# Kernel tuning notes

Measured on AMD Instinct MI355X. Metric: run time of the kernel, lower is better.

## Reference

```python
import jax, jax.numpy as jnp
import numpy as np

EMBED = 1024
HEADS = 16
HEAD_DIM = EMBED // HEADS
MAX_SEQ = 5000
THETA = 10000.0
BATCH = 16
SEQ_K = 1024
SEQ_Q = 512


def _rope_tables():
    inv = 1.0 / (THETA ** (np.arange(0, EMBED, 2)[: EMBED // 2] / EMBED))
    ang = np.outer(np.arange(MAX_SEQ), inv)  # [MAX_SEQ, EMBED//2]
    return jnp.asarray(np.cos(ang), jnp.float32), jnp.asarray(np.sin(ang), jnp.float32)

COS_T, SIN_T = _rope_tables()


def _apply_rope(x, idx):
    # x: [B, S, E]; idx: [B, S]; pairs are (x[...,2i], x[...,2i+1]) across the FULL embed dim
    B, S, E = x.shape
    xp = x.reshape(B, S, E // 2, 2)
    xr, xi = xp[..., 0], xp[..., 1]
    c, s = COS_T[idx], SIN_T[idx]  # [B, S, E//2]
    return jnp.stack([xr * c - xi * s, xr * s + xi * c], axis=-1).reshape(B, S, E)


def _attn_mask(key_padding_mask):
    # (causal triu OR key padding) AND NOT eye  (eye keeps diagonal attendable), then cut query rows
    tri = jnp.triu(jnp.ones((SEQ_K, SEQ_K), bool), k=1)
    m = jnp.logical_or(tri[None], key_padding_mask[:, None, :])  # [B, K, K]
    m = jnp.logical_and(m, ~jnp.eye(SEQ_K, dtype=bool)[None])
    return m[:, -SEQ_Q:, :]  # [B, Q, K]


def setup_inputs() -> dict:
    key = jax.random.key(0)
    ks = jax.random.split(key, 16)
    def lin(i):
        W = jax.random.normal(ks[i], (EMBED, EMBED), jnp.float32) / np.sqrt(EMBED).astype(np.float32)
        b = jnp.zeros((EMBED,), jnp.float32)
        return W, b
    Wq, bq = lin(0); Wk, bk = lin(1); Wv, bv = lin(2); Wo, bo = lin(3)
    Wxr, bxr = lin(4); Wyr, byr = lin(5)
    Wxz, bxz = lin(6); Wyz, byz = lin(7)
    Wxg, bxg = lin(8); Wyg, byg = lin(9)
    key_in = jax.random.normal(ks[10], (BATCH, SEQ_K, EMBED), jnp.float32)
    key_index = jnp.sort(jax.random.randint(ks[11], (BATCH, SEQ_K), 0, MAX_SEQ), axis=-1)
    key_padding_mask = jax.random.randint(ks[12], (BATCH, SEQ_K), 0, 2).astype(bool)
    return dict(key_in=key_in, key_index=key_index, key_padding_mask=key_padding_mask,
                Wq=Wq, bq=bq, Wk=Wk, bk=bk, Wv=Wv, bv=bv, Wo=Wo, bo=bo,
                Wxr=Wxr, bxr=bxr, Wyr=Wyr, byr=byr, Wxz=Wxz, bxz=bxz,
                Wyz=Wyz, byz=byz, Wxg=Wxg, bxg=bxg, Wyg=Wyg, byg=byg)


def reference(key_in, key_index, key_padding_mask,
              Wq, bq, Wk, bk, Wv, bv, Wo, bo,
              Wxr, bxr, Wyr, byr, Wxz, bxz, Wyz, byz, Wxg, bxg, Wyg, byg):
    B = key_in.shape[0]
    # cut_query=True: query is the last SEQ_Q steps of key
    query = key_in[:, -SEQ_Q:]
    q_idx = key_index[:, -SEQ_Q:]
    q = query @ Wq + bq
    k = key_in @ Wk + bk
    v = key_in @ Wv + bv
    # RoPE applied on full embed dim BEFORE head split (as in source)
    q = _apply_rope(q, q_idx)
    k = _apply_rope(k, key_index)
    qh = q.reshape(B, SEQ_Q, HEADS, HEAD_DIM)
    kh = k.reshape(B, SEQ_K, HEADS, HEAD_DIM)
    vh = v.reshape(B, SEQ_K, HEADS, HEAD_DIM)
    mask = _attn_mask(key_padding_mask)  # [B, Q, K]
    bias = jnp.where(mask, -jnp.inf, 0.0).astype(key_in.dtype)[:, None]  # [B,1,Q,K]
    scores = jnp.einsum('bqhd,bkhd->bhqk', qh, kh) / np.float32(np.sqrt(HEAD_DIM)) + bias
    w = jax.nn.softmax(scores, axis=-1)  # [B,H,Q,K]
    o = jnp.einsum('bhqk,bkhd->bqhd', w, vh).reshape(B, SEQ_Q, EMBED)
    o = o @ Wo + bo
    # GRU-style gated residual combine (use_residual=True, use_gated=True)
    x = query
    r = jax.nn.sigmoid(x @ Wxr + bxr + o @ Wyr + byr)
    z = jax.nn.sigmoid(x @ Wxz + bxz + o @ Wyz + byz)
    h = jnp.tanh((r * x) @ Wxg + bxg + o @ Wyg + byg)
    out = (1.0 - z) * x + z * h
    attn_weights = w.mean(axis=1)  # averaged over heads, [B, Q, K]
    return out, attn_weights
```

## Files before the change

kernel.cpp:

```cpp
#include <hip/hip_runtime.h>
#include <hip/hip_bf16.h>


typedef __attribute__((ext_vector_type(8))) short bf16x8;
typedef __attribute__((ext_vector_type(4))) float f32x4;

__device__ __forceinline__ short f2bs(float f) {
  union { __hip_bfloat16 h; short s; } u; u.h = __float2bfloat16(f); return u.s;
}

static constexpr size_t OFF_WT   = 0;
static constexpr size_t OFF_TAB  = 20971520;
static constexpr size_t OFF_XBF  = 41451520;
static constexpr size_t OFF_QH   = 75005952;
static constexpr size_t OFF_KH   = 91783168;
static constexpr size_t OFF_VT   = 125337600;
static constexpr size_t OFF_OAT  = 158892032;
static constexpr size_t OFF_O2   = 175669248;
static constexpr size_t OFF_INV  = OFF_OAT;
static constexpr size_t OFF_RBZB = 75005952;
static constexpr size_t OFF_RX   = 142114816;
static constexpr size_t OFF_HB   = OFF_XBF;

__device__ __forceinline__ int swz(int q) { return ((q & 3) << 3) ^ ((q & 12) << 2); }

__global__ __launch_bounds__(256) void k_cvtx(const float* __restrict__ x,
                                              short* __restrict__ xbf) {
  size_t i = ((size_t)blockIdx.x * 256 + threadIdx.x) * 8;
  f32x4 a = *(const f32x4*)(x + i);
  f32x4 b = *(const f32x4*)(x + i + 4);
  bf16x8 o;
  o[0] = f2bs(a[0]); o[1] = f2bs(a[1]); o[2] = f2bs(a[2]); o[3] = f2bs(a[3]);
  o[4] = f2bs(b[0]); o[5] = f2bs(b[1]); o[6] = f2bs(b[2]); o[7] = f2bs(b[3]);
  *(bf16x8*)(xbf + i) = o;
}

__global__ void k_tabinv(double* __restrict__ inv) {
  int i = threadIdx.x;
  inv[i] = pow(10000.0, -(double)i / 512.0);
}
__global__ __launch_bounds__(256) void k_table(float* __restrict__ tab,
                                               const double* __restrict__ inv) {
  int i = blockIdx.x * 256 + threadIdx.x;
  if (i >= 5000 * 512) return;
  int pos = i >> 9, fi = i & 511;
  double ds, dc;
  sincos((double)pos * inv[fi], &ds, &dc);
  tab[2 * i] = (float)dc;
  tab[2 * i + 1] = (float)ds;
}

struct W10 { const float* p[10]; };
__global__ __launch_bounds__(256) void k_wt(W10 wsrc, short* __restrict__ wt) {
  __shared__ short t[32][33];
  int kb = blockIdx.x * 32, nb = blockIdx.y * 32, wi = blockIdx.z;
  const float* src = wsrc.p[wi];
  int tid = threadIdx.x;
#pragma unroll
  for (int e = 0; e < 4; ++e) {
    int idx = e * 256 + tid;
    int kr = idx >> 5, nc = idx & 31;
    t[nc][kr] = f2bs(src[(size_t)(kb + kr) * 1024 + nb + nc]);
  }
  __syncthreads();
  short* dst = wt + (size_t)wi * 1024 * 1024;
#pragma unroll
  for (int e = 0; e < 4; ++e) {
    int idx = e * 256 + tid;
    int nr = idx >> 5, kc = idx & 31;
    dst[(size_t)(nb + nr) * 1024 + kb + kc] = t[nr][kc];
  }
}

enum { CM_BF16 = 0, CM_F32 = 2, CM_F32ACC = 3, CM_VT = 4, CM_ROPE = 5 };

template <int AMODE, int CMODE>
__global__ __launch_bounds__(256) void k_gemm(
    const short* __restrict__ A, const short* __restrict__ Bt,
    const float* __restrict__ bias, const float* __restrict__ bias2,
    void* __restrict__ Cout, int ldc,
    const float* __restrict__ tab, const int* __restrict__ kidx,
    int sshift, int qoff) {
  __shared__ __align__(16) short lA[128 * 32];
  __shared__ __align__(16) short lB[128 * 32];
  const int tid = threadIdx.x;
  const int lane = tid & 63;
  const int wv = tid >> 6;
  const int wm = wv >> 1, wn = wv & 1;
  const int lo = lane & 15, hi = lane >> 4;
  const int tm0 = blockIdx.x * 128;
  const int tn0 = blockIdx.y * 128;

  const f32x4 vz = {0.f, 0.f, 0.f, 0.f};
  f32x4 acc[4][4];
#pragma unroll
  for (int m = 0; m < 4; ++m)
#pragma unroll
    for (int n = 0; n < 4; ++n) acc[m][n] = vz;

  for (int kt = 0; kt < 32; ++kt) {
    const int k0 = kt * 32;
    __syncthreads();
#pragma unroll
    for (int i = 0; i < 2; ++i) {
      int f = i * 256 + tid;
      int r = f >> 2;
      int cb = (f & 3) * 16;
      int arow = tm0 + r;
      if (AMODE) arow = ((arow >> 9) << 10) + 512 + (arow & 511);
      const char* ga = (const char*)(A + (size_t)arow * 1024 + k0) + cb;
      __builtin_amdgcn_global_load_lds(
          (const __attribute__((address_space(1))) void*)ga,
          (__attribute__((address_space(3))) void*)((char*)lA + (size_t)(i * 256 + wv * 64) * 16),
          16, 0, 0);
      int brow = tn0 + r;
      const char* gb = (const char*)(Bt + (size_t)brow * 1024 + k0) + cb;
      __builtin_amdgcn_global_load_lds(
          (const __attribute__((address_space(1))) void*)gb,
          (__attribute__((address_space(3))) void*)((char*)lB + (size_t)(i * 256 + wv * 64) * 16),
          16, 0, 0);
    }
    __syncthreads();
    bf16x8 af[4], bfr[4];
#pragma unroll
    for (int m = 0; m < 4; ++m)
      af[m] = *(const bf16x8*)&lA[(wm * 64 + m * 16 + lo) * 32 + hi * 8];
#pragma unroll
    for (int n = 0; n < 4; ++n)
      bfr[n] = *(const bf16x8*)&lB[(wn * 64 + n * 16 + lo) * 32 + hi * 8];
#pragma unroll
    for (int m = 0; m < 4; ++m)
#pragma unroll
      for (int n = 0; n < 4; ++n)
        acc[m][n] = __builtin_amdgcn_mfma_f32_16x16x32_bf16(af[m], bfr[n], acc[m][n], 0, 0, 0);
  }

  if constexpr (CMODE == CM_ROPE) {
    __hip_bfloat16* out = (__hip_bfloat16*)Cout;
    const float2* t2 = (const float2*)tab;
    const int srows = 1 << sshift;
    const float sgn = (lane & 1) ? 1.f : -1.f;
#pragma unroll
    for (int m = 0; m < 4; ++m) {
      int row_base = tm0 + wm * 64 + m * 16 + hi * 4;
#pragma unroll
      for (int n = 0; n < 4; ++n) {
        int col = tn0 + wn * 64 + n * 16 + lo;
        float bsv = bias[col];
        int j = col >> 1, hh = col >> 6, dd = col & 63;
#pragma unroll
        for (int r = 0; r < 4; ++r) {
          int row = row_base + r;
          int bb = row >> sshift, ss = row & (srows - 1);
          int idx = kidx[bb * 1024 + qoff + ss];
          float2 cs = t2[(size_t)idx * 512 + j];
          float val = acc[m][n][r] + bsv;
          float part = __shfl_xor(val, 1);
          float rot = val * cs.x + sgn * part * cs.y;
          out[((size_t)(bb * 16 + hh) * srows + ss) * 64 + dd] = __float2bfloat16(rot);
        }
      }
    }
  } else if constexpr (CMODE == CM_VT) {
    __hip_bfloat16* out = (__hip_bfloat16*)Cout;
#pragma unroll
    for (int m = 0; m < 4; ++m) {
      int row_base = tm0 + wm * 64 + m * 16 + hi * 4;
#pragma unroll
      for (int n = 0; n < 4; ++n) {
        int col = tn0 + wn * 64 + n * 16 + lo;
        float bsv = bias[col];
        int hh = col >> 6, dd = col & 63;
#pragma unroll
        for (int r = 0; r < 4; ++r) {
          int row = row_base + r;
          int bb = row >> 10, ss = row & 1023;
          out[((size_t)(bb * 16 + hh) * 64 + dd) * 1024 + ss] =
              __float2bfloat16(acc[m][n][r] + bsv);
        }
      }
    }
  } else if constexpr (CMODE == CM_F32 || CMODE == CM_F32ACC) {
    float* out = (float*)Cout;
#pragma unroll
    for (int m = 0; m < 4; ++m) {
      int row_base = tm0 + wm * 64 + m * 16 + hi * 4;
#pragma unroll
      for (int n = 0; n < 4; ++n) {
        int col = tn0 + wn * 64 + n * 16 + lo;
        float bsv = (col < 1024 || !bias2) ? bias[col] : bias2[col - 1024];
#pragma unroll
        for (int r = 0; r < 4; ++r) {
          size_t off = (size_t)(row_base + r) * ldc + col;
          float val = acc[m][n][r] + bsv;
          if constexpr (CMODE == CM_F32ACC) val += out[off];
          out[off] = val;
        }
      }
    }
  } else {
    __hip_bfloat16* out = (__hip_bfloat16*)Cout;
#pragma unroll
    for (int m = 0; m < 4; ++m) {
      int row_base = tm0 + wm * 64 + m * 16 + hi * 4;
#pragma unroll
      for (int n = 0; n < 4; ++n) {
        int col = tn0 + wn * 64 + n * 16 + lo;
        float bsv = bias[col];
#pragma unroll
        for (int r = 0; r < 4; ++r) {
          size_t off = (size_t)(row_base + r) * ldc + col;
          out[off] = __float2bfloat16(acc[m][n][r] + bsv);
        }
      }
    }
  }
}

__global__ __launch_bounds__(512, 1) void k_attn(
    const __hip_bfloat16* __restrict__ qh,
    const __hip_bfloat16* __restrict__ kh,
    const __hip_bfloat16* __restrict__ vt,
    const unsigned char* __restrict__ padraw,
    float* __restrict__ mean_out,
    __hip_bfloat16* __restrict__ oat) {
  __shared__ float Sld[16 * 1024];
  short* Pld = (short*)Sld;
  const int wgid = blockIdx.x;
  const int b = wgid & 15, qt = wgid >> 4;
  const int tid = threadIdx.x, lane = tid & 63, wv = tid >> 6;
  const int lo = lane & 15, hi = lane >> 4;
  const int wg = wv & 3, half = wv >> 2;
  const f32x4 vz = {0.f, 0.f, 0.f, 0.f};

  auto oscw = [&](int idx) -> float& { return Sld[(idx >> 9) * 1024 + (idx & 511)]; };

  bool is_byte = false;
#pragma unroll
  for (int j = 1; j < 256; ++j)
    if ((j & 3) && padraw[j] == 1) is_byte = true;
  const int* ipad = (const int*)padraw;

  unsigned pmask = 0;
#pragma unroll
  for (int nt = 0; nt < 8; ++nt) {
    int kpos = wv * 128 + nt * 16 + lo;
    int pk = is_byte ? (int)padraw[b * 1024 + kpos]
                     : (ipad[b * 1024 + kpos] != 0 ? 1 : 0);
    pmask |= (unsigned)(pk != 0) << nt;
  }

  float macc[2][16];
#pragma unroll
  for (int rr = 0; rr < 2; ++rr)
#pragma unroll
    for (int i = 0; i < 16; ++i) macc[rr][i] = 0.f;

  const __hip_bfloat16* qbase =
      qh + ((size_t)(b * 16) * 512 + (size_t)qt * 16) * 64;
  bf16x8 qf0 = *(const bf16x8*)(qbase + (size_t)lo * 64 + hi * 8);
  bf16x8 qf1 = *(const bf16x8*)(qbase + (size_t)lo * 64 + 32 + hi * 8);

  bf16x8 kb0[8], kb1[8];
  {
    const __hip_bfloat16* kbh0 = kh + (size_t)(b * 16) * 1024 * 64;
#pragma unroll
    for (int p = 0; p < 8; ++p) {
      int kr = wv * 128 + p * 16 + lo;
      kb0[p] = *(const bf16x8*)(kbh0 + (size_t)kr * 64 + hi * 8);
      kb1[p] = *(const bf16x8*)(kbh0 + (size_t)kr * 64 + 32 + hi * 8);
    }
  }

  for (int h = 0; h < 16; ++h) {
    const __hip_bfloat16* vrow =
        vt + ((size_t)(b * 16 + h) * 64 + wg * 16 + lo) * 1024;
    const int kcg = half * 16;

    bf16x8 vbuf[16];
#pragma unroll
    for (int nt = 0; nt < 8; ++nt) {
      vbuf[2 * nt]     = *(const bf16x8*)(vrow + (kcg + 2 * nt) * 32 + hi * 8);
      vbuf[2 * nt + 1] = *(const bf16x8*)(vrow + (kcg + 2 * nt + 1) * 32 + hi * 8);
      f32x4 sa = vz;
      sa = __builtin_amdgcn_mfma_f32_16x16x32_bf16(qf0, kb0[nt], sa, 0, 0, 0);
      sa = __builtin_amdgcn_mfma_f32_16x16x32_bf16(qf1, kb1[nt], sa, 0, 0, 0);
      int kpos = wv * 128 + nt * 16 + lo;
      int pk = (pmask >> nt) & 1;
#pragma unroll
      for (int r = 0; r < 4; ++r) {
        int q = hi * 4 + r;
        int qg = 512 + qt * 16 + q;
        float sv = sa[r] * 0.125f;
        bool msk = (kpos > qg) || (kpos < qg && pk != 0);
        Sld[q * 1024 + (kpos ^ swz(q))] = msk ? -1e30f : sv;
      }
    }
    __syncthreads();

#pragma unroll
    for (int rr = 0; rr < 2; ++rr) {
      int q = wv * 2 + rr;
      const int c = swz(q);
      float* row = Sld + q * 1024;
      float v[16], mx = -1e30f;
#pragma unroll
      for (int i = 0; i < 16; ++i) {
        v[i] = row[(lane + i * 64) ^ c];
        mx = fmaxf(mx, v[i]);
      }
#pragma unroll
      for (int off = 32; off > 0; off >>= 1) mx = fmaxf(mx, __shfl_xor(mx, off));
      float sum = 0.f;
#pragma unroll
      for (int i = 0; i < 16; ++i) { v[i] = __expf(v[i] - mx); sum += v[i]; }
#pragma unroll
      for (int off = 32; off > 0; off >>= 1) sum += __shfl_xor(sum, off);
      float invs = 1.0f / sum;
      short* prow = Pld + q * 2048 + 1024;
#pragma unroll
      for (int i = 0; i < 16; ++i) {
        float p = v[i] * invs;
        prow[(lane + i * 64) ^ c] = f2bs(p);
        macc[rr][i] += p;
      }
    }
    __syncthreads();

    f32x4 oacc = vz;
    {
      const short* prow = Pld + lo * 2048 + 1024;
      const int cl = swz(lo);
      const __hip_bfloat16* kbn =
          kh + (size_t)(b * 16 + (h < 15 ? h + 1 : h)) * 1024 * 64;
#pragma unroll
      for (int kc = 0; kc < 16; ++kc) {
        if (kc < 8 && h < 15) {
          int kr = wv * 128 + kc * 16 + lo;
          kb0[kc] = *(const bf16x8*)(kbn + (size_t)kr * 64 + hi * 8);
          kb1[kc] = *(const bf16x8*)(kbn + (size_t)kr * 64 + 32 + hi * 8);
        }
        bf16x8 pa = *(const bf16x8*)&prow[((kcg + kc) * 32 + hi * 8) ^ cl];
        oacc = __builtin_amdgcn_mfma_f32_16x16x32_bf16(pa, vbuf[kc], oacc, 0, 0, 0);
      }
    }

    if (h < 15) {
      const __hip_bfloat16* qn = qbase + (size_t)(h + 1) * 512 * 64;
      qf0 = *(const bf16x8*)(qn + (size_t)lo * 64 + hi * 8);
      qf1 = *(const bf16x8*)(qn + (size_t)lo * 64 + 32 + hi * 8);
    }

    if (half == 1) {
#pragma unroll
      for (int r = 0; r < 4; ++r) oscw((wg * 64 + lane) * 4 + r) = oacc[r];
    }
    __syncthreads();
    if (half == 0) {
#pragma unroll
      for (int r = 0; r < 4; ++r) {
        float o = oacc[r] + oscw((wg * 64 + lane) * 4 + r);
        int q = qt * 16 + hi * 4 + r;
        oat[((size_t)b * 512 + q) * 1024 + h * 64 + wg * 16 + lo] =
            __float2bfloat16(o);
      }
    }
    __syncthreads();
  }

#pragma unroll
  for (int rr = 0; rr < 2; ++rr) {
    size_t mrow = ((size_t)b * 512 + (size_t)qt * 16 + wv * 2 + rr) * 1024;
#pragma unroll
    for (int i = 0; i < 16; ++i)
      mean_out[mrow + lane + i * 64] = macc[rr][i] * 0.0625f;
  }
}

__global__ __launch_bounds__(256) void k_rx(const float* __restrict__ RbZb,
                                            const float* __restrict__ x,
                                            short* __restrict__ rx) {
  size_t base = ((size_t)blockIdx.x * 256 + threadIdx.x) * 4;
  int row = (int)(base >> 10), col = (int)(base & 1023);
  int b = row >> 9, s = row & 511;
  const float* xp = x + ((size_t)(b * 1024 + 512 + s) << 10) + col;
  f32x4 rv = *(const f32x4*)(RbZb + (size_t)row * 2048 + col);
  f32x4 xv = *(const f32x4*)xp;
  typedef __attribute__((ext_vector_type(4))) short s16x4;
  s16x4 o;
#pragma unroll
  for (int j = 0; j < 4; ++j) {
    float r = 1.f / (1.f + __expf(-rv[j]));
    o[j] = f2bs(r * xv[j]);
  }
  *(s16x4*)(rx + base) = o;
}

__global__ __launch_bounds__(256) void k_final(const float* __restrict__ RbZb,
                                               const float* __restrict__ Hb,
                                               const float* __restrict__ x,
                                               float* __restrict__ out0) {
  size_t base = ((size_t)blockIdx.x * 256 + threadIdx.x) * 4;
  int row = (int)(base >> 10), col = (int)(base & 1023);
  int b = row >> 9, s = row & 511;
  const float* xp = x + ((size_t)(b * 1024 + 512 + s) << 10) + col;
  f32x4 zv = *(const f32x4*)(RbZb + (size_t)row * 2048 + 1024 + col);
  f32x4 hv = *(const f32x4*)(Hb + base);
  f32x4 xv = *(const f32x4*)xp;
  f32x4 o;
#pragma unroll
  for (int j = 0; j < 4; ++j) {
    float z = 1.f / (1.f + __expf(-zv[j]));
    float hh = tanhf(hv[j]);
    o[j] = (1.f - z) * xv[j] + z * hh;
  }
  *(f32x4*)(out0 + base) = o;
}

extern "C" void kernel_launch(void* const* d_in, const int* in_sizes, int n_in,
                              void* d_out, int out_size, void* d_ws, size_t ws_size,
                              hipStream_t stream) {
  const float* key_in = (const float*)d_in[0];
  const int* key_index = (const int*)d_in[1];
  const unsigned char* pad = (const unsigned char*)d_in[2];
  const float* bq  = (const float*)d_in[4];
  const float* bk  = (const float*)d_in[6];
  const float* bv  = (const float*)d_in[8];
  const float* bo  = (const float*)d_in[10];
  const float* bxr = (const float*)d_in[12];
  const float* byr = (const float*)d_in[14];
  const float* bxz = (const float*)d_in[16];
  const float* byz = (const float*)d_in[18];
  const float* bxg = (const float*)d_in[20];
  const float* byg = (const float*)d_in[22];

  char* ws = (char*)d_ws;
  short* wt = (short*)(ws + OFF_WT);
  float* tab = (float*)(ws + OFF_TAB);
  short* xbf = (short*)(ws + OFF_XBF);
  __hip_bfloat16* qh = (__hip_bfloat16*)(ws + OFF_QH);
  __hip_bfloat16* kh = (__hip_bfloat16*)(ws + OFF_KH);
  __hip_bfloat16* vt = (__hip_bfloat16*)(ws + OFF_VT);
  double* inv = (double*)(ws + OFF_INV);
  float* RbZb = (float*)(ws + OFF_RBZB);
  __hip_bfloat16* oat = (__hip_bfloat16*)(ws + OFF_OAT);
  short* o2 = (short*)(ws + OFF_O2);
  short* rx = (short*)(ws + OFF_RX);
  float* Hb = (float*)(ws + OFF_HB);

  float* out0 = (float*)d_out;
  float* out1 = out0 + (size_t)8388608;

  W10 wargs;
  wargs.p[0] = (const float*)d_in[3];
  wargs.p[1] = (const float*)d_in[5];
  wargs.p[2] = (const float*)d_in[7];
  wargs.p[3] = (const float*)d_in[9];
  wargs.p[4] = (const float*)d_in[11];
  wargs.p[5] = (const float*)d_in[15];
  wargs.p[6] = (const float*)d_in[13];
  wargs.p[7] = (const float*)d_in[17];
  wargs.p[8] = (const float*)d_in[19];
  wargs.p[9] = (const float*)d_in[21];

  k_cvtx<<<8192, 256, 0, stream>>>(key_in, xbf);
  k_wt<<<dim3(32, 32, 10), 256, 0, stream>>>(wargs, wt);
  k_tabinv<<<1, 512, 0, stream>>>(inv);
  k_table<<<10000, 256, 0, stream>>>(tab, inv);

  k_gemm<1, CM_ROPE><<<dim3(64, 8), 256, 0, stream>>>(
      xbf, wt + (size_t)0 * 1048576, bq, nullptr, (void*)qh, 0, tab, key_index, 9, 512);
  k_gemm<0, CM_ROPE><<<dim3(128, 8), 256, 0, stream>>>(
      xbf, wt + (size_t)1 * 1048576, bk, nullptr, (void*)kh, 0, tab, key_index, 10, 0);
  k_gemm<0, CM_VT><<<dim3(128, 8), 256, 0, stream>>>(
      xbf, wt + (size_t)2 * 1048576, bv, nullptr, (void*)vt, 0, nullptr, nullptr, 0, 0);

  k_attn<<<dim3(512), 512, 0, stream>>>(qh, kh, vt, pad, out1, oat);

  k_gemm<0, CM_BF16><<<dim3(64, 8), 256, 0, stream>>>(
      (const short*)oat, wt + (size_t)3 * 1048576, bo, nullptr, (void*)o2, 1024,
      nullptr, nullptr, 0, 0);
  k_gemm<1, CM_F32><<<dim3(64, 16), 256, 0, stream>>>(
      xbf, wt + (size_t)4 * 1048576, bxr, bxz, (void*)RbZb, 2048,
      nullptr, nullptr, 0, 0);
  k_gemm<0, CM_F32ACC><<<dim3(64, 16), 256, 0, stream>>>(
      o2, wt + (size_t)6 * 1048576, byr, byz, (void*)RbZb, 2048,
      nullptr, nullptr, 0, 0);
  k_rx<<<8192, 256, 0, stream>>>(RbZb, key_in, rx);
  k_gemm<0, CM_F32><<<dim3(64, 8), 256, 0, stream>>>(
      rx, wt + (size_t)8 * 1048576, bxg, nullptr, (void*)Hb, 1024,
      nullptr, nullptr, 0, 0);
  k_gemm<0, CM_F32ACC><<<dim3(64, 8), 256, 0, stream>>>(
      o2, wt + (size_t)9 * 1048576, byg, nullptr, (void*)Hb, 1024,
      nullptr, nullptr, 0, 0);
  k_final<<<8192, 256, 0, stream>>>(RbZb, Hb, key_in, out0);
}
```

Measured before the change: 800.8 us.

## Shrink attention workgroups to 8 query rows with streamed K/V and higher occupancy

The attention kernel now uses 256-thread workgroups over 8 query rows each, launching twice as many blocks with half the shared memory so two blocks can share a CU. K and V fragments are streamed through small double-buffered register arrays instead of being held in large register sets. The old cross-half reduction through shared memory and its extra barrier are removed. In exchange, half of each 16-row MFMA tile is wasted (hi<2 only), and every block reloads K/V per head, doubling global K/V traffic.

```diff
diff --git a/kernel.cpp b/kernel.cpp
--- a/kernel.cpp
+++ b/kernel.cpp
@@ -217,23 +217,20 @@
   }
 }
 
-__global__ __launch_bounds__(512, 1) void k_attn(
+__global__ __launch_bounds__(256, 2) void k_attn(
     const __hip_bfloat16* __restrict__ qh,
     const __hip_bfloat16* __restrict__ kh,
     const __hip_bfloat16* __restrict__ vt,
     const unsigned char* __restrict__ padraw,
     float* __restrict__ mean_out,
     __hip_bfloat16* __restrict__ oat) {
-  __shared__ float Sld[16 * 1024];
+  __shared__ float Sld[8 * 1024];
   short* Pld = (short*)Sld;
   const int wgid = blockIdx.x;
   const int b = wgid & 15, qt = wgid >> 4;
   const int tid = threadIdx.x, lane = tid & 63, wv = tid >> 6;
   const int lo = lane & 15, hi = lane >> 4;
-  const int wg = wv & 3, half = wv >> 2;
   const f32x4 vz = {0.f, 0.f, 0.f, 0.f};
-
-  auto oscw = [&](int idx) -> float& { return Sld[(idx >> 9) * 1024 + (idx & 511)]; };
 
   bool is_byte = false;
 #pragma unroll
@@ -243,8 +240,8 @@
 
   unsigned pmask = 0;
 #pragma unroll
-  for (int nt = 0; nt < 8; ++nt) {
-    int kpos = wv * 128 + nt * 16 + lo;
+  for (int nt = 0; nt < 16; ++nt) {
+    int kpos = wv * 256 + nt * 16 + lo;
     int pk = is_byte ? (int)padraw[b * 1024 + kpos]
                      : (ipad[b * 1024 + kpos] != 0 ? 1 : 0);
     pmask |= (unsigned)(pk != 0) << nt;
@@ -257,43 +254,44 @@
     for (int i = 0; i < 16; ++i) macc[rr][i] = 0.f;
 
   const __hip_bfloat16* qbase =
-      qh + ((size_t)(b * 16) * 512 + (size_t)qt * 16) * 64;
-  bf16x8 qf0 = *(const bf16x8*)(qbase + (size_t)lo * 64 + hi * 8);
-  bf16x8 qf1 = *(const bf16x8*)(qbase + (size_t)lo * 64 + 32 + hi * 8);
-
-  bf16x8 kb0[8], kb1[8];
-  {
-    const __hip_bfloat16* kbh0 = kh + (size_t)(b * 16) * 1024 * 64;
-#pragma unroll
-    for (int p = 0; p < 8; ++p) {
-      int kr = wv * 128 + p * 16 + lo;
-      kb0[p] = *(const bf16x8*)(kbh0 + (size_t)kr * 64 + hi * 8);
-      kb1[p] = *(const bf16x8*)(kbh0 + (size_t)kr * 64 + 32 + hi * 8);
-    }
-  }
+      qh + ((size_t)(b * 16) * 512 + (size_t)qt * 8) * 64;
+  bf16x8 qf0 = *(const bf16x8*)(qbase + (size_t)(lo & 7) * 64 + hi * 8);
+  bf16x8 qf1 = *(const bf16x8*)(qbase + (size_t)(lo & 7) * 64 + 32 + hi * 8);
 
   for (int h = 0; h < 16; ++h) {
+    const __hip_bfloat16* kbh = kh + (size_t)(b * 16 + h) * 1024 * 64;
     const __hip_bfloat16* vrow =
-        vt + ((size_t)(b * 16 + h) * 64 + wg * 16 + lo) * 1024;
-    const int kcg = half * 16;
-
-    bf16x8 vbuf[16];
-#pragma unroll
-    for (int nt = 0; nt < 8; ++nt) {
-      vbuf[2 * nt]     = *(const bf16x8*)(vrow + (kcg + 2 * nt) * 32 + hi * 8);
-      vbuf[2 * nt + 1] = *(const bf16x8*)(vrow + (kcg + 2 * nt + 1) * 32 + hi * 8);
+        vt + ((size_t)(b * 16 + h) * 64 + wv * 16 + lo) * 1024;
+
+    bf16x8 kbuf[2][2];
+#pragma unroll
+    for (int p = 0; p < 2; ++p) {
+      int kr = wv * 256 + p * 16 + lo;
+      kbuf[p][0] = *(const bf16x8*)(kbh + (size_t)kr * 64 + hi * 8);
+      kbuf[p][1] = *(const bf16x8*)(kbh + (size_t)kr * 64 + 32 + hi * 8);
+    }
+#pragma unroll
+    for (int nt = 0; nt < 16; ++nt) {
+      bf16x8 ck0 = kbuf[nt & 1][0], ck1 = kbuf[nt & 1][1];
+      if (nt < 14) {
+        int kr = wv * 256 + (nt + 2) * 16 + lo;
+        kbuf[nt & 1][0] = *(const bf16x8*)(kbh + (size_t)kr * 64 + hi * 8);
+        kbuf[nt & 1][1] = *(const bf16x8*)(kbh + (size_t)kr * 64 + 32 + hi * 8);
+      }
       f32x4 sa = vz;
-      sa = __builtin_amdgcn_mfma_f32_16x16x32_bf16(qf0, kb0[nt], sa, 0, 0, 0);
-      sa = __builtin_amdgcn_mfma_f32_16x16x32_bf16(qf1, kb1[nt], sa, 0, 0, 0);
-      int kpos = wv * 128 + nt * 16 + lo;
+      sa = __builtin_amdgcn_mfma_f32_16x16x32_bf16(qf0, ck0, sa, 0, 0, 0);
+      sa = __builtin_amdgcn_mfma_f32_16x16x32_bf16(qf1, ck1, sa, 0, 0, 0);
+      int kpos = wv * 256 + nt * 16 + lo;
       int pk = (pmask >> nt) & 1;
-#pragma unroll
-      for (int r = 0; r < 4; ++r) {
-        int q = hi * 4 + r;
-        int qg = 512 + qt * 16 + q;
-        float sv = sa[r] * 0.125f;
-        bool msk = (kpos > qg) || (kpos < qg && pk != 0);
-        Sld[q * 1024 + (kpos ^ swz(q))] = msk ? -1e30f : sv;
+      if (hi < 2) {
+#pragma unroll
+        for (int r = 0; r < 4; ++r) {
+          int q = hi * 4 + r;
+          int qg = 512 + qt * 8 + q;
+          float sv = sa[r] * 0.125f;
+          bool msk = (kpos > qg) || (kpos < qg && pk != 0);
+          Sld[q * 1024 + (kpos ^ swz(q))] = msk ? -1e30f : sv;
+        }
       }
     }
     __syncthreads();
@@ -329,48 +327,42 @@
 
     f32x4 oacc = vz;
     {
-      const short* prow = Pld + lo * 2048 + 1024;
-      const int cl = swz(lo);
-      const __hip_bfloat16* kbn =
-          kh + (size_t)(b * 16 + (h < 15 ? h + 1 : h)) * 1024 * 64;
-#pragma unroll
-      for (int kc = 0; kc < 16; ++kc) {
-        if (kc < 8 && h < 15) {
-          int kr = wv * 128 + kc * 16 + lo;
-          kb0[kc] = *(const bf16x8*)(kbn + (size_t)kr * 64 + hi * 8);
-          kb1[kc] = *(const bf16x8*)(kbn + (size_t)kr * 64 + 32 + hi * 8);
-        }
-        bf16x8 pa = *(const bf16x8*)&prow[((kcg + kc) * 32 + hi * 8) ^ cl];
-        oacc = __builtin_amdgcn_mfma_f32_16x16x32_bf16(pa, vbuf[kc], oacc, 0, 0, 0);
+      const short* prow = Pld + (lo & 7) * 2048 + 1024;
+      const int cl = swz(lo & 7);
+      bf16x8 vbuf[2];
+#pragma unroll
+      for (int p = 0; p < 2; ++p)
+        vbuf[p] = *(const bf16x8*)(vrow + p * 32 + hi * 8);
+#pragma unroll
+      for (int kc = 0; kc < 32; ++kc) {
+        bf16x8 cv = vbuf[kc & 1];
+        if (kc < 30)
+          vbuf[kc & 1] = *(const bf16x8*)(vrow + (kc + 2) * 32 + hi * 8);
+        bf16x8 pa = *(const bf16x8*)&prow[(kc * 32 + hi * 8) ^ cl];
+        oacc = __builtin_amdgcn_mfma_f32_16x16x32_bf16(pa, cv, oacc, 0, 0, 0);
       }
     }
 
     if (h < 15) {
       const __hip_bfloat16* qn = qbase + (size_t)(h + 1) * 512 * 64;
-      qf0 = *(const bf16x8*)(qn + (size_t)lo * 64 + hi * 8);
-      qf1 = *(const bf16x8*)(qn + (size_t)lo * 64 + 32 + hi * 8);
-    }
-
-    if (half == 1) {
-#pragma unroll
-      for (int r = 0; r < 4; ++r) oscw((wg * 64 + lane) * 4 + r) = oacc[r];
+      qf0 = *(const bf16x8*)(qn + (size_t)(lo & 7) * 64 + hi * 8);
+      qf1 = *(const bf16x8*)(qn + (size_t)(lo & 7) * 64 + 32 + hi * 8);
+    }
+
+    if (hi < 2) {
+#pragma unroll
+      for (int r = 0; r < 4; ++r) {
+        int q = qt * 8 + hi * 4 + r;
+        oat[((size_t)b * 512 + q) * 1024 + h * 64 + wv * 16 + lo] =
+            __float2bfloat16(oacc[r]);
+      }
     }
     __syncthreads();
-    if (half == 0) {
-#pragma unroll
-      for (int r = 0; r < 4; ++r) {
-        float o = oacc[r] + oscw((wg * 64 + lane) * 4 + r);
-        int q = qt * 16 + hi * 4 + r;
-        oat[((size_t)b * 512 + q) * 1024 + h * 64 + wg * 16 + lo] =
-            __float2bfloat16(o);
-      }
-    }
-    __syncthreads();
   }
 
 #pragma unroll
   for (int rr = 0; rr < 2; ++rr) {
-    size_t mrow = ((size_t)b * 512 + (size_t)qt * 16 + wv * 2 + rr) * 1024;
+    size_t mrow = ((size_t)b * 512 + (size_t)qt * 8 + wv * 2 + rr) * 1024;
 #pragma unroll
     for (int i = 0; i < 16; ++i)
       mean_out[mrow + lane + i * 64] = macc[rr][i] * 0.0625f;
@@ -475,7 +467,7 @@
   k_gemm<0, CM_VT><<<dim3(128, 8), 256, 0, stream>>>(
       xbf, wt + (size_t)2 * 1048576, bv, nullptr, (void*)vt, 0, nullptr, nullptr, 0, 0);
 
-  k_attn<<<dim3(512), 512, 0, stream>>>(qh, kh, vt, pad, out1, oat);
+  k_attn<<<dim3(1024), 256, 0, stream>>>(qh, kh, vt, pad, out1, oat);
 
   k_gemm<0, CM_BF16><<<dim3(64, 8), 256, 0, stream>>>(
       (const short*)oat, wt + (size_t)3 * 1048576, bo, nullptr, (void*)o2, 1024,
```

Measured after the change: 983.6 us. +22.8%, slower.
